# Kernel tuning notes

Measured on AMD Instinct MI355X. Metric: run time of the kernel, lower is better.

The kernel has to match this reference:

```python
import jax, jax.numpy as jnp
import numpy as np

N = 32768
E = 262144
OUT = 512
H = 8
DH = OUT // H


def setup_inputs() -> dict:
    key = jax.random.key(0)
    ks = jax.random.split(key, 12)
    s = 0.02
    return {
        "h": jax.random.normal(ks[0], (N, 512), dtype=jnp.float32),
        "row": jax.random.randint(ks[1], (E,), 0, N, dtype=jnp.int32),
        "col": jax.random.randint(ks[2], (E,), 0, N, dtype=jnp.int32),
        "W_in": jax.random.normal(ks[3], (512, OUT), dtype=jnp.float32) * s,
        "b_in": jnp.zeros((OUT,), dtype=jnp.float32),
        "W_q": jax.random.normal(ks[4], (OUT, OUT), dtype=jnp.float32) * s,
        "b_q": jnp.zeros((OUT,), dtype=jnp.float32),
        "W_k": jax.random.normal(ks[5], (OUT, OUT), dtype=jnp.float32) * s,
        "b_k": jnp.zeros((OUT,), dtype=jnp.float32),
        "W_v": jax.random.normal(ks[6], (OUT, OUT), dtype=jnp.float32) * s,
        "b_v": jnp.zeros((OUT,), dtype=jnp.float32),
    }


def reference(h, row, col, W_in, b_in, W_q, b_q, W_k, b_k, W_v, b_v):
    scaling = DH ** -0.5
    x = h @ W_in + b_in                                   # [N, OUT]
    q = ((x @ W_q + b_q) * scaling).reshape(N, H, DH)     # [N, H, DH]
    k = (x @ W_k + b_k).reshape(N, H, DH)
    v = (x @ W_v + b_v).reshape(N, H, DH)

    # bsddmm: per-edge, per-head attention logits only at adjacency nonzeros
    logits = jnp.einsum("ehd,ehd->eh", q[row], k[col])    # [E, H]

    # sparse row-wise softmax over each node's incident edges
    m = jax.ops.segment_max(logits, row, num_segments=N)  # [N, H]
    ex = jnp.exp(logits - m[row])                         # [E, H]
    denom = jax.ops.segment_sum(ex, row, num_segments=N)  # [N, H]
    attn = ex / denom[row]                                # [E, H]

    # bspmm: aggregate v over neighbors with sparse attention weights
    out = jax.ops.segment_sum(attn[:, :, None] * v[col], row, num_segments=N)  # [N, H, DH]
    return out
```

## Files before the change

### kernel.cpp

```cpp
#include <hip/hip_runtime.h>

#define NN 32768
#define EE 262144
#define DM 512
#define NQKV 1536
#define NHEAD 8
#define DHEAD 64

typedef unsigned short u16;
typedef unsigned int u32;
typedef __attribute__((ext_vector_type(8))) short bf16x8;
typedef __attribute__((ext_vector_type(4))) float f32x4;
typedef __attribute__((ext_vector_type(8))) u16 u16x8;
typedef __attribute__((ext_vector_type(4))) u32 u32x4;

__device__ __forceinline__ float bf2f(u16 u) {
  union { u32 i; float f; } x; x.i = ((u32)u) << 16; return x.f;
}
__device__ __forceinline__ float bflo(u32 p) {
  union { u32 i; float f; } x; x.i = p << 16; return x.f;
}
__device__ __forceinline__ float bfhi(u32 p) {
  union { u32 i; float f; } x; x.i = p & 0xFFFF0000u; return x.f;
}
__device__ __forceinline__ u16 f2bf(float f) {
  union { float f; u32 i; } x; x.f = f;
  u32 r = x.i + 0x7FFFu + ((x.i >> 16) & 1u);
  return (u16)(r >> 16);
}

__device__ __forceinline__ void load_lds16(const u16* g, u16* l) {
  __builtin_amdgcn_global_load_lds(
      (const __attribute__((address_space(1))) char*)(const void*)g,
      (__attribute__((address_space(3))) char*)(void*)l, 16, 0, 0);
}

__device__ __forceinline__ int swz(int r, int s) {
  return s ^ (r & 3) ^ ((r >> 2) & 1);
}


__global__ void tcast_w(const float* __restrict__ Wq, const float* __restrict__ Wk,
                        const float* __restrict__ Wv, u16* __restrict__ At) {
  const int z = blockIdx.z;
  const float* W = (z == 0) ? Wq : (z == 1) ? Wk : Wv;
  const float scale = (z == 0) ? 0.125f : 1.0f;
  const int m0 = blockIdx.x * 64;
  const int j0 = blockIdx.y * 64;
  __shared__ float t[64][65];
  const int tx = threadIdx.x & 63, ty = threadIdx.x >> 6;
#pragma unroll
  for (int i = 0; i < 16; ++i) {
    const int r = ty * 16 + i;
    t[r][tx] = W[(size_t)(m0 + r) * 512 + (j0 + tx)];
  }
  __syncthreads();
#pragma unroll
  for (int i = 0; i < 16; ++i) {
    const int j = j0 + ty * 16 + i;
    const int pr = (z == 0) ? j : (512 + 2 * j + (z - 1));
    At[(size_t)pr * 512 + (m0 + tx)] = f2bf(t[tx][ty * 16 + i] * scale);
  }
}

__global__ void cast_win(const float* __restrict__ Win, u16* __restrict__ Winb) {
  const int i = (blockIdx.x * 256 + threadIdx.x) * 8;
  float4 a = *(const float4*)&Win[i];
  float4 b = *(const float4*)&Win[i + 4];
  u16x8 o = { f2bf(a.x), f2bf(a.y), f2bf(a.z), f2bf(a.w),
              f2bf(b.x), f2bf(b.y), f2bf(b.z), f2bf(b.w) };
  *(u16x8*)&Winb[i] = o;
}

__global__ void make_bias(const float* __restrict__ bin,
                          const float* __restrict__ Wq, const float* __restrict__ bq,
                          const float* __restrict__ Wk, const float* __restrict__ bk,
                          const float* __restrict__ Wv, const float* __restrict__ bv,
                          float* __restrict__ bias) {
  const int j = blockIdx.x * 256 + threadIdx.x;
  if (j >= 1536) return;
  const float* Wsel; const float* bsel; int jj; float scale = 1.0f; int pos;
  if (j < 512)       { Wsel = Wq; bsel = bq; jj = j;        scale = 0.125f; pos = j; }
  else if (j < 1024) { Wsel = Wk; bsel = bk; jj = j - 512;  pos = 512 + 2 * jj; }
  else               { Wsel = Wv; bsel = bv; jj = j - 1024; pos = 513 + 2 * jj; }
  float s = 0.f;
  for (int m = 0; m < 512; ++m) s = fmaf(bin[m], Wsel[m * 512 + jj], s);
  bias[pos] = (s + bsel[jj]) * scale;
}

__global__ void cast_h(const float* __restrict__ h, u16* __restrict__ hb) {
  const int i = (blockIdx.x * 256 + threadIdx.x) * 8;
  float4 a = *(const float4*)&h[i];
  float4 b = *(const float4*)&h[i + 4];
  u16x8 o = { f2bf(a.x), f2bf(a.y), f2bf(a.z), f2bf(a.w),
              f2bf(b.x), f2bf(b.y), f2bf(b.z), f2bf(b.w) };
  *(u16x8*)&hb[i] = o;
}

__global__ void count_deg(const int* __restrict__ row, int* __restrict__ deg) {
  const int e = blockIdx.x * 256 + threadIdx.x;
  atomicAdd(&deg[row[e]], 1);
}

__global__ void scan_deg(const int* __restrict__ deg, int* __restrict__ row_ptr,
                         int* __restrict__ cursor) {
  __shared__ int sums[1024];
  const int t = threadIdx.x;
  const int base = t * 32;
  int loc[32];
  int s = 0;
#pragma unroll
  for (int i = 0; i < 32; ++i) { loc[i] = s; s += deg[base + i]; }
  sums[t] = s;
  __syncthreads();
  for (int off = 1; off < 1024; off <<= 1) {
    int v = (t >= off) ? sums[t - off] : 0;
    __syncthreads();
    sums[t] += v;
    __syncthreads();
  }
  const int excl = sums[t] - s;
#pragma unroll
  for (int i = 0; i < 32; ++i) {
    const int val = excl + loc[i];
    row_ptr[base + i] = val;
    cursor[base + i] = val;
  }
  if (t == 1023) row_ptr[NN] = sums[1023];
}

__global__ void fill_csr(const int* __restrict__ row, const int* __restrict__ col,
                         int* __restrict__ cursor, int* __restrict__ dst) {
  const int e = blockIdx.x * 256 + threadIdx.x;
  const int r = row[e];
  const int p = atomicAdd(&cursor[r], 1);
  dst[p] = col[e];
}

__global__ __launch_bounds__(256, 2) void gemm_wt(
    const u16* __restrict__ A,
    const u16* __restrict__ B,
    u16* __restrict__ C) {
  __shared__ u16 As[2][128 * 32];
  __shared__ u16 Bs[2][128 * 32];
  const int tid = threadIdx.x;
  const int lane = tid & 63;
  const int wave = tid >> 6;
  const int quad = lane >> 4;
  const int l16 = lane & 15;
  const int m0 = blockIdx.y * 128;
  const int n0 = blockIdx.x * 128;
  const int wm = (wave >> 1) * 64;
  const int wn = (wave & 1) * 64;

  const int c0 = tid, c1 = tid + 256;
  const int r0 = c0 >> 2, ko0 = swz(r0, c0 & 3) * 8;
  const int r1 = c1 >> 2, ko1 = swz(r1, c1 & 3) * 8;
  const u16* Ag0 = A + (size_t)(m0 + r0) * DM + ko0;
  const u16* Ag1 = A + (size_t)(m0 + r1) * DM + ko1;
  const u16* Bg0 = B + (size_t)(n0 + r0) * DM + ko0;
  const u16* Bg1 = B + (size_t)(n0 + r1) * DM + ko1;

  f32x4 acc[4][4];
#pragma unroll
  for (int i = 0; i < 4; ++i)
#pragma unroll
    for (int j = 0; j < 4; ++j) acc[i][j] = (f32x4){0.f, 0.f, 0.f, 0.f};

  load_lds16(Ag0, &As[0][c0 * 8]);
  load_lds16(Bg0, &Bs[0][c0 * 8]);
  load_lds16(Ag1, &As[0][c1 * 8]);
  load_lds16(Bg1, &Bs[0][c1 * 8]);
  __syncthreads();

  int cur = 0;
#pragma unroll
  for (int kt = 32; kt < DM; kt += 32) {
    load_lds16(Ag0 + kt, &As[cur ^ 1][c0 * 8]);
    load_lds16(Bg0 + kt, &Bs[cur ^ 1][c0 * 8]);
    load_lds16(Ag1 + kt, &As[cur ^ 1][c1 * 8]);
    load_lds16(Bg1 + kt, &Bs[cur ^ 1][c1 * 8]);
    bf16x8 a[4], b[4];
#pragma unroll
    for (int i = 0; i < 4; ++i) {
      const int ra = wm + i * 16 + l16;
      const int rb = wn + i * 16 + l16;
      a[i] = *(const bf16x8*)&As[cur][ra * 32 + swz(ra, quad) * 8];
      b[i] = *(const bf16x8*)&Bs[cur][rb * 32 + swz(rb, quad) * 8];
    }
#pragma unroll
    for (int mi = 0; mi < 4; ++mi)
#pragma unroll
      for (int ni = 0; ni < 4; ++ni)
        acc[mi][ni] = __builtin_amdgcn_mfma_f32_16x16x32_bf16(a[mi], b[ni], acc[mi][ni], 0, 0, 0);
    __syncthreads();
    cur ^= 1;
  }
  {
    bf16x8 a[4], b[4];
#pragma unroll
    for (int i = 0; i < 4; ++i) {
      const int ra = wm + i * 16 + l16;
      const int rb = wn + i * 16 + l16;
      a[i] = *(const bf16x8*)&As[cur][ra * 32 + swz(ra, quad) * 8];
      b[i] = *(const bf16x8*)&Bs[cur][rb * 32 + swz(rb, quad) * 8];
    }
#pragma unroll
    for (int mi = 0; mi < 4; ++mi)
#pragma unroll
      for (int ni = 0; ni < 4; ++ni)
        acc[mi][ni] = __builtin_amdgcn_mfma_f32_16x16x32_bf16(a[mi], b[ni], acc[mi][ni], 0, 0, 0);
  }

#pragma unroll
  for (int ni = 0; ni < 4; ++ni) {
    const int coln = n0 + wn + ni * 16 + l16;
#pragma unroll
    for (int mi = 0; mi < 4; ++mi) {
#pragma unroll
      for (int r = 0; r < 4; ++r) {
        const int rowm = m0 + wm + mi * 16 + quad * 4 + r;
        C[(size_t)rowm * 512 + coln] = f2bf(acc[mi][ni][r]);
      }
    }
  }
}

__global__ __launch_bounds__(256, 2) void gemm_qkv(
    const u16* __restrict__ A,
    const u16* __restrict__ B,
    const float* __restrict__ bias,
    u16* __restrict__ C) {
  __shared__ u16 As[2][128 * 32];
  __shared__ u16 Bs[2][128 * 32];
  const int tid = threadIdx.x;
  const int lane = tid & 63;
  const int wave = tid >> 6;
  const int quad = lane >> 4;
  const int l16 = lane & 15;

  const int bid = blockIdx.y * 12 + blockIdx.x;
  const int sw = (bid & 7) * 384 + (bid >> 3);
  const int bx = sw % 12;
  const int by = sw / 12;
  const int m0 = by * 128;
  const int n0 = bx * 128;
  const int wm = (wave >> 1) * 64;
  const int wn = (wave & 1) * 64;

  const int c0 = tid, c1 = tid + 256;
  const int r0 = c0 >> 2, ko0 = swz(r0, c0 & 3) * 8;
  const int r1 = c1 >> 2, ko1 = swz(r1, c1 & 3) * 8;
  const u16* Ag0 = A + (size_t)(m0 + r0) * DM + ko0;
  const u16* Ag1 = A + (size_t)(m0 + r1) * DM + ko1;
  const u16* Bg0 = B + (size_t)(n0 + r0) * DM + ko0;
  const u16* Bg1 = B + (size_t)(n0 + r1) * DM + ko1;

  f32x4 acc[4][4];
#pragma unroll
  for (int i = 0; i < 4; ++i)
#pragma unroll
    for (int j = 0; j < 4; ++j) acc[i][j] = (f32x4){0.f, 0.f, 0.f, 0.f};

  load_lds16(Ag0, &As[0][c0 * 8]);
  load_lds16(Bg0, &Bs[0][c0 * 8]);
  load_lds16(Ag1, &As[0][c1 * 8]);
  load_lds16(Bg1, &Bs[0][c1 * 8]);
  __syncthreads();

  int cur = 0;
#pragma unroll
  for (int kt = 32; kt < DM; kt += 32) {
    load_lds16(Ag0 + kt, &As[cur ^ 1][c0 * 8]);
    load_lds16(Bg0 + kt, &Bs[cur ^ 1][c0 * 8]);
    load_lds16(Ag1 + kt, &As[cur ^ 1][c1 * 8]);
    load_lds16(Bg1 + kt, &Bs[cur ^ 1][c1 * 8]);
    bf16x8 a[4], b[4];
#pragma unroll
    for (int i = 0; i < 4; ++i) {
      const int ra = wm + i * 16 + l16;
      const int rb = wn + i * 16 + l16;
      a[i] = *(const bf16x8*)&As[cur][ra * 32 + swz(ra, quad) * 8];
      b[i] = *(const bf16x8*)&Bs[cur][rb * 32 + swz(rb, quad) * 8];
    }
#pragma unroll
    for (int mi = 0; mi < 4; ++mi)
#pragma unroll
      for (int ni = 0; ni < 4; ++ni)
        acc[mi][ni] = __builtin_amdgcn_mfma_f32_16x16x32_bf16(a[mi], b[ni], acc[mi][ni], 0, 0, 0);
    __syncthreads();
    cur ^= 1;
  }
  {
    bf16x8 a[4], b[4];
#pragma unroll
    for (int i = 0; i < 4; ++i) {
      const int ra = wm + i * 16 + l16;
      const int rb = wn + i * 16 + l16;
      a[i] = *(const bf16x8*)&As[cur][ra * 32 + swz(ra, quad) * 8];
      b[i] = *(const bf16x8*)&Bs[cur][rb * 32 + swz(rb, quad) * 8];
    }
#pragma unroll
    for (int mi = 0; mi < 4; ++mi)
#pragma unroll
      for (int ni = 0; ni < 4; ++ni)
        acc[mi][ni] = __builtin_amdgcn_mfma_f32_16x16x32_bf16(a[mi], b[ni], acc[mi][ni], 0, 0, 0);
  }

#pragma unroll
  for (int ni = 0; ni < 4; ++ni) {
    const int coln = n0 + wn + ni * 16 + l16;
    const float bv = bias[coln];
#pragma unroll
    for (int mi = 0; mi < 4; ++mi) {
#pragma unroll
      for (int r = 0; r < 4; ++r) {
        const int rowm = m0 + wm + mi * 16 + quad * 4 + r;
        C[(size_t)rowm * NQKV + coln] = f2bf(acc[mi][ni][r] + bv);
      }
    }
  }
}

__global__ __launch_bounds__(256) void attn_agg(
    const u16* __restrict__ qkv16, const u32* __restrict__ qkv32,
    const int* __restrict__ row_ptr, const int* __restrict__ dst,
    float* __restrict__ out) {
  const int gt = blockIdx.x * 256 + threadIdx.x;
  const int node = gt >> 6;
  const int lane = gt & 63;
  const u16x8 qr = *(const u16x8*)&qkv16[(size_t)node * NQKV + lane * 8];
  float qf[8];
#pragma unroll
  for (int j = 0; j < 8; ++j) qf[j] = bf2f(qr[j]);

  const int beg = row_ptr[node];
  const int end = row_ptr[node + 1];
  float acc[8] = {0.f,0.f,0.f,0.f,0.f,0.f,0.f,0.f};
  float denom = 0.f;

  for (int e = beg; e < end; e += 4) {
    u32 p[4][8];
    int idx[4];
#pragma unroll
    for (int jj = 0; jj < 4; ++jj) {
      const int ee = min(e + jj, end - 1);
      idx[jj] = dst[ee];
    }
#pragma unroll
    for (int jj = 0; jj < 4; ++jj) {
      const u32* pp = qkv32 + (size_t)idx[jj] * 768 + 256 + lane * 8;
      *(u32x4*)&p[jj][0] = *(const u32x4*)pp;
      *(u32x4*)&p[jj][4] = *(const u32x4*)(pp + 4);
    }
#pragma unroll
    for (int jj = 0; jj < 4; ++jj) {
      float s = 0.f;
#pragma unroll
      for (int j = 0; j < 8; ++j) s = fmaf(qf[j], bflo(p[jj][j]), s);
      s += __shfl_xor(s, 1, 64);
      s += __shfl_xor(s, 2, 64);
      s += __shfl_xor(s, 4, 64);
      const float ex = (e + jj < end) ? __expf(s) : 0.f;
      denom += ex;
#pragma unroll
      for (int j = 0; j < 8; ++j) acc[j] = fmaf(ex, bfhi(p[jj][j]), acc[j]);
    }
  }

  const float inv = (end > beg) ? (1.0f / denom) : 0.f;
  float4 o0 = { acc[0] * inv, acc[1] * inv, acc[2] * inv, acc[3] * inv };
  float4 o1 = { acc[4] * inv, acc[5] * inv, acc[6] * inv, acc[7] * inv };
  float* op = &out[(size_t)node * 512 + lane * 8];
  *(float4*)op = o0;
  *(float4*)(op + 4) = o1;
}

extern "C" void kernel_launch(void* const* d_in, const int* in_sizes, int n_in,
                              void* d_out, int out_size, void* d_ws, size_t ws_size,
                              hipStream_t stream) {
  const float* h   = (const float*)d_in[0];
  const int*   row = (const int*)d_in[1];
  const int*   col = (const int*)d_in[2];
  const float* Win = (const float*)d_in[3];
  const float* bin = (const float*)d_in[4];
  const float* Wq  = (const float*)d_in[5];
  const float* bq  = (const float*)d_in[6];
  const float* Wk  = (const float*)d_in[7];
  const float* bk  = (const float*)d_in[8];
  const float* Wv  = (const float*)d_in[9];
  const float* bv  = (const float*)d_in[10];
  float* out = (float*)d_out;

  char* ws = (char*)d_ws;
  u16*   qkv     = (u16*)(ws + 0);
  u16*   hb      = (u16*)(ws + 100663296);
  u16*   Wt      = (u16*)(ws + 134217728);
  float* bias    = (float*)(ws + 135790592);
  int*   deg     = (int*)(ws + 135796736);
  int*   row_ptr = (int*)(ws + 135927808);
  int*   cursor  = (int*)(ws + 136058888);
  int*   dst     = (int*)(ws + 136189960);
  u16*   At      = (u16*)(ws + 0);
  u16*   Winb    = (u16*)(ws + 1572864);

  (void)hipMemsetAsync(deg, 0, NN * sizeof(int), stream);
  hipLaunchKernelGGL(tcast_w,   dim3(8, 8, 3), dim3(256), 0, stream, Wq, Wk, Wv, At);
  hipLaunchKernelGGL(cast_win,  dim3((512 * 512 / 8) / 256), dim3(256), 0, stream, Win, Winb);
  hipLaunchKernelGGL(make_bias, dim3(6), dim3(256), 0, stream, bin, Wq, bq, Wk, bk, Wv, bv, bias);
  hipLaunchKernelGGL(cast_h,    dim3((NN * DM / 8) / 256), dim3(256), 0, stream, h, hb);
  hipLaunchKernelGGL(count_deg, dim3(EE / 256), dim3(256), 0, stream, row, deg);
  hipLaunchKernelGGL(scan_deg,  dim3(1), dim3(1024), 0, stream, deg, row_ptr, cursor);
  hipLaunchKernelGGL(fill_csr,  dim3(EE / 256), dim3(256), 0, stream, row, col, cursor, dst);
  hipLaunchKernelGGL(gemm_wt,   dim3(512 / 128, 1536 / 128), dim3(256), 0, stream, At, Winb, Wt);
  hipLaunchKernelGGL(gemm_qkv,  dim3(NQKV / 128, NN / 128), dim3(256), 0, stream, hb, Wt, bias, qkv);
  hipLaunchKernelGGL(attn_agg,  dim3((NN * 64) / 256), dim3(256), 0, stream,
                     qkv, (const u32*)qkv, row_ptr, dst, out);
}
```

Measured before the change: 370.4 us.

## Enlarge QKV GEMM tiles with 4-stage LDS pipeline; prefetch edge indices in attention

The QKV GEMM moves from 128x128 tiles with 256 threads and double buffering to 256x256 tiles with 512 threads, a four-stage LDS ring filled two steps ahead, split A/B loads interleaved with MFMA halves, and s_setprio around the MFMA blocks. This aims to hide global-load latency better and raise arithmetic intensity, at the cost of 128KB of LDS per block and fewer blocks in the grid. The attention kernel now keeps the node index in a scalar register, prefetches the next four neighbor indices while processing the current four, and handles the tail edges in a separate scalar loop without masking.

```diff
diff --git a/kernel.cpp b/kernel.cpp
--- a/kernel.cpp
+++ b/kernel.cpp
@@ -38,7 +38,6 @@
 __device__ __forceinline__ int swz(int r, int s) {
   return s ^ (r & 3) ^ ((r >> 2) & 1);
 }
-
 
 __global__ void tcast_w(const float* __restrict__ Wq, const float* __restrict__ Wk,
                         const float* __restrict__ Wv, u16* __restrict__ At) {
@@ -226,97 +225,122 @@
   }
 }
 
-__global__ __launch_bounds__(256, 2) void gemm_qkv(
+#define BKQ 32
+__global__ __launch_bounds__(512, 2) void gemm_qkv(
     const u16* __restrict__ A,
     const u16* __restrict__ B,
     const float* __restrict__ bias,
     u16* __restrict__ C) {
-  __shared__ u16 As[2][128 * 32];
-  __shared__ u16 Bs[2][128 * 32];
+  __shared__ u16 As[4][256 * BKQ];
+  __shared__ u16 Bs[4][256 * BKQ];
   const int tid = threadIdx.x;
   const int lane = tid & 63;
   const int wave = tid >> 6;
   const int quad = lane >> 4;
   const int l16 = lane & 15;
-
-  const int bid = blockIdx.y * 12 + blockIdx.x;
-  const int sw = (bid & 7) * 384 + (bid >> 3);
-  const int bx = sw % 12;
-  const int by = sw / 12;
-  const int m0 = by * 128;
-  const int n0 = bx * 128;
-  const int wm = (wave >> 1) * 64;
-  const int wn = (wave & 1) * 64;
-
-  const int c0 = tid, c1 = tid + 256;
-  const int r0 = c0 >> 2, ko0 = swz(r0, c0 & 3) * 8;
-  const int r1 = c1 >> 2, ko1 = swz(r1, c1 & 3) * 8;
-  const u16* Ag0 = A + (size_t)(m0 + r0) * DM + ko0;
-  const u16* Ag1 = A + (size_t)(m0 + r1) * DM + ko1;
-  const u16* Bg0 = B + (size_t)(n0 + r0) * DM + ko0;
-  const u16* Bg1 = B + (size_t)(n0 + r1) * DM + ko1;
-
-  f32x4 acc[4][4];
-#pragma unroll
-  for (int i = 0; i < 4; ++i)
+  const int wr = wave >> 2;
+  const int wc = wave & 3;
+
+  const int bid = blockIdx.y * 6 + blockIdx.x;
+  const int sw = (bid & 7) * 96 + (bid >> 3);
+  const int bx = sw % 6, by = sw / 6;
+  const int m0 = by * 256, n0 = bx * 256;
+
+  const int sa0 = tid, sa1 = tid + 512;
+  const int ra0 = sa0 >> 2, ca0 = (sa0 & 3) ^ ((ra0 >> 1) & 3);
+  const int ra1 = sa1 >> 2, ca1 = (sa1 & 3) ^ ((ra1 >> 1) & 3);
+  const u16* Aga = A + (size_t)(m0 + ra0) * DM + ca0 * 8;
+  const u16* Agb = A + (size_t)(m0 + ra1) * DM + ca1 * 8;
+  const u16* Bga = B + (size_t)(n0 + ra0) * DM + ca0 * 8;
+  const u16* Bgb = B + (size_t)(n0 + ra1) * DM + ca1 * 8;
+
+  int offA[8], offB[4];
+#pragma unroll
+  for (int mf = 0; mf < 8; ++mf) {
+    const int r = wr * 128 + mf * 16 + l16;
+    offA[mf] = r * BKQ + (quad ^ ((r >> 1) & 3)) * 8;
+  }
+#pragma unroll
+  for (int nf = 0; nf < 4; ++nf) {
+    const int r = wc * 64 + nf * 16 + l16;
+    offB[nf] = r * BKQ + (quad ^ ((r >> 1) & 3)) * 8;
+  }
+
+  f32x4 acc[8][4];
+#pragma unroll
+  for (int i = 0; i < 8; ++i)
 #pragma unroll
     for (int j = 0; j < 4; ++j) acc[i][j] = (f32x4){0.f, 0.f, 0.f, 0.f};
 
-  load_lds16(Ag0, &As[0][c0 * 8]);
-  load_lds16(Bg0, &Bs[0][c0 * 8]);
-  load_lds16(Ag1, &As[0][c1 * 8]);
-  load_lds16(Bg1, &Bs[0][c1 * 8]);
-  __syncthreads();
-
-  int cur = 0;
-#pragma unroll
-  for (int kt = 32; kt < DM; kt += 32) {
-    load_lds16(Ag0 + kt, &As[cur ^ 1][c0 * 8]);
-    load_lds16(Bg0 + kt, &Bs[cur ^ 1][c0 * 8]);
-    load_lds16(Ag1 + kt, &As[cur ^ 1][c1 * 8]);
-    load_lds16(Bg1 + kt, &Bs[cur ^ 1][c1 * 8]);
+  load_lds16(Aga, &As[0][sa0 * 8]);
+  load_lds16(Agb, &As[0][sa1 * 8]);
+  load_lds16(Bga, &Bs[0][sa0 * 8]);
+  load_lds16(Bgb, &Bs[0][sa1 * 8]);
+  load_lds16(Aga + BKQ, &As[1][sa0 * 8]);
+  load_lds16(Agb + BKQ, &As[1][sa1 * 8]);
+  load_lds16(Bga + BKQ, &Bs[1][sa0 * 8]);
+  load_lds16(Bgb + BKQ, &Bs[1][sa1 * 8]);
+  asm volatile("s_waitcnt vmcnt(4)\n\ts_barrier" ::: "memory");
+
+  for (int t = 0; t < 16; ++t) {
+    const int bt = t & 3;
+    const u16* Al = &As[bt][0];
+    const u16* Bl = &Bs[bt][0];
+    const int kg = (t + 2) * BKQ;
     bf16x8 a[4], b[4];
-#pragma unroll
-    for (int i = 0; i < 4; ++i) {
-      const int ra = wm + i * 16 + l16;
-      const int rb = wn + i * 16 + l16;
-      a[i] = *(const bf16x8*)&As[cur][ra * 32 + swz(ra, quad) * 8];
-      b[i] = *(const bf16x8*)&Bs[cur][rb * 32 + swz(rb, quad) * 8];
-    }
+
+#pragma unroll
+    for (int i = 0; i < 4; ++i) a[i] = *(const bf16x8*)&Al[offA[i]];
+#pragma unroll
+    for (int i = 0; i < 4; ++i) b[i] = *(const bf16x8*)&Bl[offB[i]];
+    if (t < 14) {
+      const int b2 = (t + 2) & 3;
+      load_lds16(Aga + kg, &As[b2][sa0 * 8]);
+      load_lds16(Agb + kg, &As[b2][sa1 * 8]);
+    }
+    __builtin_amdgcn_s_barrier();
+    __builtin_amdgcn_s_setprio(1);
 #pragma unroll
     for (int mi = 0; mi < 4; ++mi)
 #pragma unroll
       for (int ni = 0; ni < 4; ++ni)
         acc[mi][ni] = __builtin_amdgcn_mfma_f32_16x16x32_bf16(a[mi], b[ni], acc[mi][ni], 0, 0, 0);
-    __syncthreads();
-    cur ^= 1;
-  }
-  {
-    bf16x8 a[4], b[4];
-#pragma unroll
-    for (int i = 0; i < 4; ++i) {
-      const int ra = wm + i * 16 + l16;
-      const int rb = wn + i * 16 + l16;
-      a[i] = *(const bf16x8*)&As[cur][ra * 32 + swz(ra, quad) * 8];
-      b[i] = *(const bf16x8*)&Bs[cur][rb * 32 + swz(rb, quad) * 8];
-    }
+    __builtin_amdgcn_s_setprio(0);
+    __builtin_amdgcn_s_barrier();
+
+#pragma unroll
+    for (int i = 0; i < 4; ++i) a[i] = *(const bf16x8*)&Al[offA[4 + i]];
+    if (t < 14) {
+      const int b2 = (t + 2) & 3;
+      load_lds16(Bga + kg, &Bs[b2][sa0 * 8]);
+      load_lds16(Bgb + kg, &Bs[b2][sa1 * 8]);
+    }
+    __builtin_amdgcn_s_barrier();
+    __builtin_amdgcn_s_setprio(1);
 #pragma unroll
     for (int mi = 0; mi < 4; ++mi)
 #pragma unroll
       for (int ni = 0; ni < 4; ++ni)
-        acc[mi][ni] = __builtin_amdgcn_mfma_f32_16x16x32_bf16(a[mi], b[ni], acc[mi][ni], 0, 0, 0);
-  }
-
-#pragma unroll
-  for (int ni = 0; ni < 4; ++ni) {
-    const int coln = n0 + wn + ni * 16 + l16;
+        acc[4 + mi][ni] = __builtin_amdgcn_mfma_f32_16x16x32_bf16(a[mi], b[ni], acc[4 + mi][ni], 0, 0, 0);
+    __builtin_amdgcn_s_setprio(0);
+
+    if (t < 14) {
+      asm volatile("s_waitcnt vmcnt(4)\n\ts_barrier" ::: "memory");
+    } else if (t == 14) {
+      asm volatile("s_waitcnt vmcnt(0)\n\ts_barrier" ::: "memory");
+    }
+  }
+
+#pragma unroll
+  for (int nf = 0; nf < 4; ++nf) {
+    const int coln = n0 + wc * 64 + nf * 16 + l16;
     const float bv = bias[coln];
 #pragma unroll
-    for (int mi = 0; mi < 4; ++mi) {
+    for (int mf = 0; mf < 8; ++mf) {
 #pragma unroll
       for (int r = 0; r < 4; ++r) {
-        const int rowm = m0 + wm + mi * 16 + quad * 4 + r;
-        C[(size_t)rowm * NQKV + coln] = f2bf(acc[mi][ni][r] + bv);
+        const int rowm = m0 + wr * 128 + mf * 16 + quad * 4 + r;
+        C[(size_t)rowm * NQKV + coln] = f2bf(acc[mf][nf][r] + bv);
       }
     }
   }
@@ -327,8 +351,9 @@
     const int* __restrict__ row_ptr, const int* __restrict__ dst,
     float* __restrict__ out) {
   const int gt = blockIdx.x * 256 + threadIdx.x;
-  const int node = gt >> 6;
   const int lane = gt & 63;
+  const int node = __builtin_amdgcn_readfirstlane(gt >> 6);
+
   const u16x8 qr = *(const u16x8*)&qkv16[(size_t)node * NQKV + lane * 8];
   float qf[8];
 #pragma unroll
@@ -339,33 +364,56 @@
   float acc[8] = {0.f,0.f,0.f,0.f,0.f,0.f,0.f,0.f};
   float denom = 0.f;
 
-  for (int e = beg; e < end; e += 4) {
-    u32 p[4][8];
+  int e = beg;
+  if (e + 4 <= end) {
     int idx[4];
 #pragma unroll
-    for (int jj = 0; jj < 4; ++jj) {
-      const int ee = min(e + jj, end - 1);
-      idx[jj] = dst[ee];
-    }
-#pragma unroll
-    for (int jj = 0; jj < 4; ++jj) {
-      const u32* pp = qkv32 + (size_t)idx[jj] * 768 + 256 + lane * 8;
-      *(u32x4*)&p[jj][0] = *(const u32x4*)pp;
-      *(u32x4*)&p[jj][4] = *(const u32x4*)(pp + 4);
-    }
-#pragma unroll
-    for (int jj = 0; jj < 4; ++jj) {
-      float s = 0.f;
-#pragma unroll
-      for (int j = 0; j < 8; ++j) s = fmaf(qf[j], bflo(p[jj][j]), s);
-      s += __shfl_xor(s, 1, 64);
-      s += __shfl_xor(s, 2, 64);
-      s += __shfl_xor(s, 4, 64);
-      const float ex = (e + jj < end) ? __expf(s) : 0.f;
-      denom += ex;
-#pragma unroll
-      for (int j = 0; j < 8; ++j) acc[j] = fmaf(ex, bfhi(p[jj][j]), acc[j]);
-    }
+    for (int jj = 0; jj < 4; ++jj) idx[jj] = dst[e + jj];
+    for (; e + 4 <= end; e += 4) {
+      const int lim = end - 1;
+      int idxn[4];
+#pragma unroll
+      for (int jj = 0; jj < 4; ++jj) idxn[jj] = dst[min(e + 4 + jj, lim)];
+      u32 p[4][8];
+#pragma unroll
+      for (int jj = 0; jj < 4; ++jj) {
+        const u32* pp = qkv32 + (size_t)idx[jj] * 768 + 256 + lane * 8;
+        *(u32x4*)&p[jj][0] = *(const u32x4*)pp;
+        *(u32x4*)&p[jj][4] = *(const u32x4*)(pp + 4);
+      }
+#pragma unroll
+      for (int jj = 0; jj < 4; ++jj) {
+        float s = 0.f;
+#pragma unroll
+        for (int j = 0; j < 8; ++j) s = fmaf(qf[j], bflo(p[jj][j]), s);
+        s += __shfl_xor(s, 1, 64);
+        s += __shfl_xor(s, 2, 64);
+        s += __shfl_xor(s, 4, 64);
+        const float ex = __expf(s);
+        denom += ex;
+#pragma unroll
+        for (int j = 0; j < 8; ++j) acc[j] = fmaf(ex, bfhi(p[jj][j]), acc[j]);
+      }
+#pragma unroll
+      for (int jj = 0; jj < 4; ++jj) idx[jj] = idxn[jj];
+    }
+  }
+  for (; e < end; ++e) {
+    const int id = dst[e];
+    const u32* pp = qkv32 + (size_t)id * 768 + 256 + lane * 8;
+    u32 p[8];
+    *(u32x4*)&p[0] = *(const u32x4*)pp;
+    *(u32x4*)&p[4] = *(const u32x4*)(pp + 4);
+    float s = 0.f;
+#pragma unroll
+    for (int j = 0; j < 8; ++j) s = fmaf(qf[j], bflo(p[j]), s);
+    s += __shfl_xor(s, 1, 64);
+    s += __shfl_xor(s, 2, 64);
+    s += __shfl_xor(s, 4, 64);
+    const float ex = __expf(s);
+    denom += ex;
+#pragma unroll
+    for (int j = 0; j < 8; ++j) acc[j] = fmaf(ex, bfhi(p[j]), acc[j]);
   }
 
   const float inv = (end > beg) ? (1.0f / denom) : 0.f;
@@ -413,7 +461,7 @@
   hipLaunchKernelGGL(scan_deg,  dim3(1), dim3(1024), 0, stream, deg, row_ptr, cursor);
   hipLaunchKernelGGL(fill_csr,  dim3(EE / 256), dim3(256), 0, stream, row, col, cursor, dst);
   hipLaunchKernelGGL(gemm_wt,   dim3(512 / 128, 1536 / 128), dim3(256), 0, stream, At, Winb, Wt);
-  hipLaunchKernelGGL(gemm_qkv,  dim3(NQKV / 128, NN / 128), dim3(256), 0, stream, hb, Wt, bias, qkv);
+  hipLaunchKernelGGL(gemm_qkv,  dim3(NQKV / 256, NN / 256), dim3(512), 0, stream, hb, Wt, bias, qkv);
   hipLaunchKernelGGL(attn_agg,  dim3((NN * 64) / 256), dim3(256), 0, stream,
                      qkv, (const u32*)qkv, row_ptr, dst, out);
 }
```

Result: slower. 385.3 us (+4.0%).

## Fuse prep kernels into one launch, split bias GEMV, deepen edge unroll

Applied to the files above, without the earlier changes.

Merges the five preprocessing kernels (h cast, W_in cast, degree count, weight transpose-cast, bias GEMV) into a single block-dispatched kernel, which removes launch gaps. The bias GEMV is now split over 16 chunks of the reduction dimension and combined with atomics into a pre-zeroed buffer, giving it more parallelism than the old 6-block serial loop. The attention aggregation now processes 8 gathered edges per iteration instead of 4 to keep more loads in flight, at the cost of higher register pressure and more wasted work on low-degree nodes. It also needs an extra memset and makes the bias sum order non-deterministic.

```diff
diff --git a/kernel.cpp b/kernel.cpp
--- a/kernel.cpp
+++ b/kernel.cpp
@@ -39,67 +39,91 @@
   return s ^ (r & 3) ^ ((r >> 2) & 1);
 }
 
-
-__global__ void tcast_w(const float* __restrict__ Wq, const float* __restrict__ Wk,
-                        const float* __restrict__ Wv, u16* __restrict__ At) {
-  const int z = blockIdx.z;
-  const float* W = (z == 0) ? Wq : (z == 1) ? Wk : Wv;
-  const float scale = (z == 0) ? 0.125f : 1.0f;
-  const int m0 = blockIdx.x * 64;
-  const int j0 = blockIdx.y * 64;
+#define GB_CASTH 8192
+#define GB_CASTW 128
+#define GB_CNTD  1024
+#define GB_TCW   192
+#define GB_BIAS  96
+__global__ void prep_all(const float* __restrict__ h, u16* __restrict__ hb,
+                         const float* __restrict__ Win, u16* __restrict__ Winb,
+                         const int* __restrict__ row, int* __restrict__ deg,
+                         const float* __restrict__ Wq, const float* __restrict__ Wk,
+                         const float* __restrict__ Wv, u16* __restrict__ At,
+                         const float* __restrict__ bin, const float* __restrict__ bq,
+                         const float* __restrict__ bk, const float* __restrict__ bv,
+                         float* __restrict__ bias) {
   __shared__ float t[64][65];
-  const int tx = threadIdx.x & 63, ty = threadIdx.x >> 6;
-#pragma unroll
-  for (int i = 0; i < 16; ++i) {
-    const int r = ty * 16 + i;
-    t[r][tx] = W[(size_t)(m0 + r) * 512 + (j0 + tx)];
-  }
-  __syncthreads();
-#pragma unroll
-  for (int i = 0; i < 16; ++i) {
-    const int j = j0 + ty * 16 + i;
-    const int pr = (z == 0) ? j : (512 + 2 * j + (z - 1));
-    At[(size_t)pr * 512 + (m0 + tx)] = f2bf(t[tx][ty * 16 + i] * scale);
-  }
-}
-
-__global__ void cast_win(const float* __restrict__ Win, u16* __restrict__ Winb) {
-  const int i = (blockIdx.x * 256 + threadIdx.x) * 8;
-  float4 a = *(const float4*)&Win[i];
-  float4 b = *(const float4*)&Win[i + 4];
-  u16x8 o = { f2bf(a.x), f2bf(a.y), f2bf(a.z), f2bf(a.w),
-              f2bf(b.x), f2bf(b.y), f2bf(b.z), f2bf(b.w) };
-  *(u16x8*)&Winb[i] = o;
-}
-
-__global__ void make_bias(const float* __restrict__ bin,
-                          const float* __restrict__ Wq, const float* __restrict__ bq,
-                          const float* __restrict__ Wk, const float* __restrict__ bk,
-                          const float* __restrict__ Wv, const float* __restrict__ bv,
-                          float* __restrict__ bias) {
-  const int j = blockIdx.x * 256 + threadIdx.x;
-  if (j >= 1536) return;
-  const float* Wsel; const float* bsel; int jj; float scale = 1.0f; int pos;
-  if (j < 512)       { Wsel = Wq; bsel = bq; jj = j;        scale = 0.125f; pos = j; }
-  else if (j < 1024) { Wsel = Wk; bsel = bk; jj = j - 512;  pos = 512 + 2 * jj; }
-  else               { Wsel = Wv; bsel = bv; jj = j - 1024; pos = 513 + 2 * jj; }
-  float s = 0.f;
-  for (int m = 0; m < 512; ++m) s = fmaf(bin[m], Wsel[m * 512 + jj], s);
-  bias[pos] = (s + bsel[jj]) * scale;
-}
-
-__global__ void cast_h(const float* __restrict__ h, u16* __restrict__ hb) {
-  const int i = (blockIdx.x * 256 + threadIdx.x) * 8;
-  float4 a = *(const float4*)&h[i];
-  float4 b = *(const float4*)&h[i + 4];
-  u16x8 o = { f2bf(a.x), f2bf(a.y), f2bf(a.z), f2bf(a.w),
-              f2bf(b.x), f2bf(b.y), f2bf(b.z), f2bf(b.w) };
-  *(u16x8*)&hb[i] = o;
-}
-
-__global__ void count_deg(const int* __restrict__ row, int* __restrict__ deg) {
-  const int e = blockIdx.x * 256 + threadIdx.x;
-  atomicAdd(&deg[row[e]], 1);
+  const int tid = threadIdx.x;
+  int b = blockIdx.x;
+
+  if (b < GB_CASTH) {
+    const int i = (b * 256 + tid) * 8;
+    float4 a = *(const float4*)&h[i];
+    float4 c = *(const float4*)&h[i + 4];
+    u16x8 o = { f2bf(a.x), f2bf(a.y), f2bf(a.z), f2bf(a.w),
+                f2bf(c.x), f2bf(c.y), f2bf(c.z), f2bf(c.w) };
+    *(u16x8*)&hb[i] = o;
+    return;
+  }
+  b -= GB_CASTH;
+  if (b < GB_CASTW) {
+    const int i = (b * 256 + tid) * 8;
+    float4 a = *(const float4*)&Win[i];
+    float4 c = *(const float4*)&Win[i + 4];
+    u16x8 o = { f2bf(a.x), f2bf(a.y), f2bf(a.z), f2bf(a.w),
+                f2bf(c.x), f2bf(c.y), f2bf(c.z), f2bf(c.w) };
+    *(u16x8*)&Winb[i] = o;
+    return;
+  }
+  b -= GB_CASTW;
+  if (b < GB_CNTD) {
+    const int e = b * 256 + tid;
+    atomicAdd(&deg[row[e]], 1);
+    return;
+  }
+  b -= GB_CNTD;
+  if (b < GB_TCW) {
+    const int z = b / 64;
+    const int r64 = b % 64;
+    const float* W = (z == 0) ? Wq : (z == 1) ? Wk : Wv;
+    const float scale = (z == 0) ? 0.125f : 1.0f;
+    const int m0 = (r64 >> 3) * 64;
+    const int j0 = (r64 & 7) * 64;
+    const int tx = tid & 63, ty = tid >> 6;
+#pragma unroll
+    for (int i = 0; i < 16; ++i) {
+      const int r = ty * 16 + i;
+      t[r][tx] = W[(size_t)(m0 + r) * 512 + (j0 + tx)];
+    }
+    __syncthreads();
+#pragma unroll
+    for (int i = 0; i < 16; ++i) {
+      const int j = j0 + ty * 16 + i;
+      const int pr = (z == 0) ? j : (512 + 2 * j + (z - 1));
+      At[(size_t)pr * 512 + (m0 + tx)] = f2bf(t[tx][ty * 16 + i] * scale);
+    }
+    return;
+  }
+  b -= GB_TCW;
+  {
+    const int j = (b % 6) * 256 + tid;
+    const int m0 = (b / 6) * 32;
+    const float* Wsel; const float* bsel; int jj; float scale = 1.0f; int pos;
+    if (j < 512)       { Wsel = Wq; bsel = bq; jj = j;        scale = 0.125f; pos = j; }
+    else if (j < 1024) { Wsel = Wk; bsel = bk; jj = j - 512;  pos = 512 + 2 * jj; }
+    else               { Wsel = Wv; bsel = bv; jj = j - 1024; pos = 513 + 2 * jj; }
+    float s0 = 0.f, s1 = 0.f, s2 = 0.f, s3 = 0.f;
+#pragma unroll
+    for (int m = 0; m < 32; m += 4) {
+      s0 = fmaf(bin[m0 + m],     Wsel[(size_t)(m0 + m)     * 512 + jj], s0);
+      s1 = fmaf(bin[m0 + m + 1], Wsel[(size_t)(m0 + m + 1) * 512 + jj], s1);
+      s2 = fmaf(bin[m0 + m + 2], Wsel[(size_t)(m0 + m + 2) * 512 + jj], s2);
+      s3 = fmaf(bin[m0 + m + 3], Wsel[(size_t)(m0 + m + 3) * 512 + jj], s3);
+    }
+    float add = ((s0 + s1) + (s2 + s3)) * scale;
+    if (m0 == 0) add += bsel[jj] * scale;
+    atomicAdd(&bias[pos], add);
+  }
 }
 
 __global__ void scan_deg(const int* __restrict__ deg, int* __restrict__ row_ptr,
@@ -329,39 +353,38 @@
   const int gt = blockIdx.x * 256 + threadIdx.x;
   const int node = gt >> 6;
   const int lane = gt & 63;
+  const int beg = row_ptr[node];
+  const int end = row_ptr[node + 1];
+
   const u16x8 qr = *(const u16x8*)&qkv16[(size_t)node * NQKV + lane * 8];
   float qf[8];
 #pragma unroll
   for (int j = 0; j < 8; ++j) qf[j] = bf2f(qr[j]);
 
-  const int beg = row_ptr[node];
-  const int end = row_ptr[node + 1];
   float acc[8] = {0.f,0.f,0.f,0.f,0.f,0.f,0.f,0.f};
   float denom = 0.f;
 
-  for (int e = beg; e < end; e += 4) {
-    u32 p[4][8];
-    int idx[4];
-#pragma unroll
-    for (int jj = 0; jj < 4; ++jj) {
-      const int ee = min(e + jj, end - 1);
-      idx[jj] = dst[ee];
-    }
-#pragma unroll
-    for (int jj = 0; jj < 4; ++jj) {
+  for (int e = beg; e < end; e += 8) {
+    const int lim = end - 1;
+    int idx[8];
+#pragma unroll
+    for (int jj = 0; jj < 8; ++jj) idx[jj] = dst[min(e + jj, lim)];
+    u32 p[8][8];
+#pragma unroll
+    for (int jj = 0; jj < 8; ++jj) {
       const u32* pp = qkv32 + (size_t)idx[jj] * 768 + 256 + lane * 8;
       *(u32x4*)&p[jj][0] = *(const u32x4*)pp;
       *(u32x4*)&p[jj][4] = *(const u32x4*)(pp + 4);
     }
 #pragma unroll
-    for (int jj = 0; jj < 4; ++jj) {
+    for (int jj = 0; jj < 8; ++jj) {
       float s = 0.f;
 #pragma unroll
       for (int j = 0; j < 8; ++j) s = fmaf(qf[j], bflo(p[jj][j]), s);
       s += __shfl_xor(s, 1, 64);
       s += __shfl_xor(s, 2, 64);
       s += __shfl_xor(s, 4, 64);
-      const float ex = (e + jj < end) ? __expf(s) : 0.f;
+      const float ex = (e + jj <= lim) ? __expf(s) : 0.f;
       denom += ex;
 #pragma unroll
       for (int j = 0; j < 8; ++j) acc[j] = fmaf(ex, bfhi(p[jj][j]), acc[j]);
@@ -405,11 +428,12 @@
   u16*   Winb    = (u16*)(ws + 1572864);
 
   (void)hipMemsetAsync(deg, 0, NN * sizeof(int), stream);
-  hipLaunchKernelGGL(tcast_w,   dim3(8, 8, 3), dim3(256), 0, stream, Wq, Wk, Wv, At);
-  hipLaunchKernelGGL(cast_win,  dim3((512 * 512 / 8) / 256), dim3(256), 0, stream, Win, Winb);
-  hipLaunchKernelGGL(make_bias, dim3(6), dim3(256), 0, stream, bin, Wq, bq, Wk, bk, Wv, bv, bias);
-  hipLaunchKernelGGL(cast_h,    dim3((NN * DM / 8) / 256), dim3(256), 0, stream, h, hb);
-  hipLaunchKernelGGL(count_deg, dim3(EE / 256), dim3(256), 0, stream, row, deg);
+  (void)hipMemsetAsync(bias, 0, NQKV * sizeof(float), stream);
+  hipLaunchKernelGGL(prep_all,
+                     dim3(GB_CASTH + GB_CASTW + GB_CNTD + GB_TCW + GB_BIAS),
+                     dim3(256), 0, stream,
+                     h, hb, Win, Winb, row, deg, Wq, Wk, Wv, At,
+                     bin, bq, bk, bv, bias);
   hipLaunchKernelGGL(scan_deg,  dim3(1), dim3(1024), 0, stream, deg, row_ptr, cursor);
   hipLaunchKernelGGL(fill_csr,  dim3(EE / 256), dim3(256), 0, stream, row, col, cursor, dst);
   hipLaunchKernelGGL(gemm_wt,   dim3(512 / 128, 1536 / 128), dim3(256), 0, stream, At, Winb, Wt);
```

New measurement: 339.7 us. 1.09x faster.
